# Kernel tuning notes

Hardware: AMD Instinct MI355X
Metric: run time of the kernel (lower is better)

The kernel has to match this reference:

```python
import jax, jax.numpy as jnp
import numpy as np

B, N, IN_D = 4, 2046, 512
D, H = 1024, 16
DH = D // H  # 64
S = N + 2
EPS = 1e-5


def setup_inputs() -> dict:
    key = jax.random.key(0)
    ks = jax.random.split(key, 9)
    s = lambda k, shp, fan: jax.random.normal(k, shp, jnp.float32) * (1.0 / np.sqrt(fan))
    return {
        "x": jax.random.normal(ks[0], (B, N, IN_D), jnp.float32),
        "W_map": s(ks[1], (IN_D, D), IN_D),
        "b_map": jnp.zeros((D,), jnp.float32),
        "time_token": jax.random.normal(ks[2], (1, D), jnp.float32),
        "cluster_token": jax.random.normal(ks[3], (1, D), jnp.float32),
        "ln_g": jnp.ones((D,), jnp.float32),
        "ln_b": jnp.zeros((D,), jnp.float32),
        "Wq": s(ks[4], (H, DH, DH), DH),
        "bq": jax.random.normal(ks[5], (H, DH), jnp.float32) * 0.01,
        "Wk": s(ks[6], (H, DH, DH), DH),
        "bk": jax.random.normal(ks[7], (H, DH), jnp.float32) * 0.01,
    }


def reference(x, W_map, b_map, time_token, cluster_token, ln_g, ln_b, Wq, bq, Wk, bk):
    b = x.shape[0]
    tokens = x @ W_map + b_map                       # [B, N, D]
    tt = jnp.broadcast_to(time_token[None], (b, 1, D))
    ct = jnp.broadcast_to(cluster_token[None], (b, 1, D))
    out = jnp.concatenate([tt, ct, tokens], axis=1)  # [B, S, D]
    # LayerNorm (norm1)
    mu = jnp.mean(out, axis=-1, keepdims=True)
    var = jnp.mean(jnp.square(out - mu), axis=-1, keepdims=True)
    h = (out - mu) * jax.lax.rsqrt(var + EPS) * ln_g + ln_b
    # MSAAttention: per-head Q/K linear, softmax(QK^T / sqrt(d_head))
    hh = h.reshape(b, S, H, DH)
    q = jnp.einsum("bshd,hde->bhse", hh, Wq) + bq[None, :, None, :]
    k = jnp.einsum("bshd,hde->bhse", hh, Wk) + bk[None, :, None, :]
    scores = jnp.einsum("bhse,bhte->bhst", q, k) / np.sqrt(DH).astype(np.float32)
    attn = jax.nn.softmax(scores, axis=-1)           # [B, H, S, S]
    # hstack over heads -> [B, S, H*S]; extract_attention reshapes back and
    # means over heads, then takes rows 0 (timing) and 1 (id).
    m = jnp.mean(attn, axis=1)                       # [B, S, S]
    return m[:, 0, :], m[:, 1, :]
```

## Files before the change

kernel.cpp:

```cpp
#include <hip/hip_runtime.h>
#include <hip/hip_bf16.h>
#include <math.h>

#define BB 4
#define NN 2046
#define IND 512
#define DD 1024
#define HH 16
#define SS 2048
#define MM (BB*NN)
#define MPAD 8192
#define ROWPAD 8256
#define EPSV 1e-5f

#define OFF_U    0
#define OFF_G    2048
#define OFF_C2   2080
#define OFF_S12  4096
#define OFF_A    (4096 + 2*ROWPAD)
#define OFF_XH_B  1139200
#define OFF_WHT_B (OFF_XH_B + MPAD*IND*2)
#define OFF_WLT_B (OFF_WHT_B + DD*IND*2)

typedef float f32x4 __attribute__((ext_vector_type(4)));
typedef __bf16 bf16x8 __attribute__((ext_vector_type(8)));
typedef unsigned short u16x8 __attribute__((ext_vector_type(8)));

__device__ __forceinline__ unsigned short f2bf_rne(float f) {
  unsigned int u = __float_as_uint(f);
  u += 0x7FFFu + ((u >> 16) & 1u);
  return (unsigned short)(u >> 16);
}

__device__ __forceinline__ float waveSum(float v) {
  #pragma unroll
  for (int m = 32; m >= 1; m >>= 1) v += __shfl_xor(v, m, 64);
  return v;
}

__device__ __forceinline__ float blockReduceSum(float v, volatile float* buf4) {
  #pragma unroll
  for (int m = 32; m >= 1; m >>= 1) v += __shfl_xor(v, m, 64);
  int wid = threadIdx.x >> 6;
  __syncthreads();
  if ((threadIdx.x & 63) == 0) buf4[wid] = v;
  __syncthreads();
  return buf4[0] + buf4[1] + buf4[2] + buf4[3];
}

#define GLOAD_LDS16(g, l) \
  __builtin_amdgcn_global_load_lds((const __attribute__((address_space(1))) void*)(g), \
                                   (__attribute__((address_space(3))) void*)(l), 16, 0, 0)

__global__ __launch_bounds__(256) void prep(
    const float* __restrict__ x, const float* __restrict__ Wm,
    const float* __restrict__ tt, const float* __restrict__ ct,
    const float* __restrict__ lng, const float* __restrict__ lnb,
    const float* __restrict__ Wq, const float* __restrict__ bq,
    const float* __restrict__ Wk, const float* __restrict__ bk,
    unsigned short* __restrict__ xh, unsigned short* __restrict__ wht,
    unsigned short* __restrict__ wlt, float* __restrict__ ws,
    float* __restrict__ out) {
  __shared__ float tile[64][65];
  __shared__ float hq[4][64];
  __shared__ float qs[4][64];
  const int bid = blockIdx.x;
  const int t = threadIdx.x;

  if (bid < 2048) {
    const int row = bid * 4 + (t >> 6);
    const int c0 = (t & 63) * 8;
    const size_t po = (size_t)row * IND + c0;
    u16x8 hv;
    if (row < MM) {
      const float4* xv = (const float4*)(x + po);
      float4 a = xv[0], b = xv[1];
      float vv[8] = {a.x, a.y, a.z, a.w, b.x, b.y, b.z, b.w};
      #pragma unroll
      for (int i = 0; i < 8; ++i) hv[i] = f2bf_rne(vv[i]);
    } else {
      #pragma unroll
      for (int i = 0; i < 8; ++i) hv[i] = 0;
    }
    *(u16x8*)(xh + po) = hv;
  } else if (bid < 2176) {
    const int b2 = bid - 2048;
    const int kb = b2 >> 4, nb = b2 & 15;
    const int k0 = kb * 64, n0 = nb * 64;
    #pragma unroll
    for (int q = 0; q < 16; ++q) {
      int lin = q * 256 + t;
      int kk = lin >> 6, nn = lin & 63;
      tile[kk][nn] = Wm[(size_t)(k0 + kk) * DD + n0 + nn];
    }
    __syncthreads();
    #pragma unroll
    for (int q = 0; q < 16; ++q) {
      int lin = q * 256 + t;
      int nn = lin >> 6, kk = lin & 63;
      float v = tile[kk][nn];
      unsigned short hh = f2bf_rne(v);
      wht[(size_t)(n0 + nn) * IND + k0 + kk] = hh;
      wlt[(size_t)(n0 + nn) * IND + k0 + kk] =
          f2bf_rne(v - __uint_as_float(((unsigned int)hh) << 16));
    }
  } else if (bid < 2184) {
    const int w = t >> 6, e = t & 63;
    const int sh = (bid - 2176) * 4 + w;
    const int s = sh >> 4, h = sh & 15;
    const float* src = s ? ct : tt;
    float* U   = ws + OFF_U;
    float* s12 = ws + OFF_S12;
    float* Ap  = ws + OFF_A;

    float s1 = 0.f, s2 = 0.f;
    #pragma unroll
    for (int i = 0; i < 16; ++i) { float v = src[i*64 + e]; s1 += v; s2 += v*v; }
    s1 = waveSum(s1); s2 = waveSum(s2);
    if (h == 0 && e == 0) {
      s12[(MPAD + s)*2 + 0] = s1;
      s12[(MPAD + s)*2 + 1] = s2;
    }
    const float mu = s1 * (1.f/DD);
    const float var = s2 * (1.f/DD) - mu*mu;
    const float rstd = rsqrtf(var + EPSV);
    const int d0 = h * 64;
    hq[w][e] = (src[d0+e] - mu) * rstd * lng[d0+e] + lnb[d0+e];
    float qv = bq[d0+e];
    #pragma unroll 8
    for (int d = 0; d < 64; ++d) qv += hq[w][d] * Wq[(size_t)(d0+d)*64 + e];
    qs[w][e] = qv;
    float wt = 0.f;
    #pragma unroll 8
    for (int ee = 0; ee < 64; ++ee) wt += Wk[(size_t)(d0+e)*64 + ee] * qs[w][ee];
    wt *= 0.125f;
    const float c = waveSum(qs[w][e] * bk[d0+e]) * 0.125f;
    const float u = lng[d0+e] * wt;
    U[s*DD + d0 + e] = u;
    const float G  = waveSum(lng[d0+e] * wt);
    const float C  = waveSum(lnb[d0+e] * wt);
    const float a0 = waveSum(tt[d0+e] * u);
    const float a1 = waveSum(ct[d0+e] * u);
    if (e == 0) {
      ws[OFF_G  + sh] = G;
      ws[OFF_C2 + sh] = C + c;
      Ap[(size_t)sh*ROWPAD + MPAD + 0] = a0;
      Ap[(size_t)sh*ROWPAD + MPAD + 1] = a1;
    }
  } else if (bid < 2252) {
    const int j = (bid - 2184) * 4096 + t * 16;
    const float4 z = make_float4(0.f, 0.f, 0.f, 0.f);
    #pragma unroll
    for (int q = 0; q < 4; ++q) {
      const int f = j + q * 4;
      if (f < 16384) {
        *(float4*)(ws + OFF_S12 + f) = z;
      } else {
        const int g = f - 16384;
        const int sl = g >> 13, rw = g & 8191;
        *(float4*)(ws + OFF_A + (size_t)sl*ROWPAD + rw) = z;
      }
    }
  } else {
    const int f = (bid - 2252) * 4096 + t * 16;
    const float4 z = make_float4(0.f, 0.f, 0.f, 0.f);
    #pragma unroll
    for (int q = 0; q < 4; ++q) *(float4*)(out + f + q*4) = z;
  }
}

__global__ __launch_bounds__(256, 2) void stageB(
    const unsigned short* __restrict__ xh,
    const unsigned short* __restrict__ wht, const unsigned short* __restrict__ wlt,
    const float* __restrict__ bmap, float* __restrict__ ws) {
  __shared__ unsigned short Ash[128*64], Bsh[128*64], Bsl[128*64];
  __shared__ float s12w[4][64][2];
  __shared__ float aw[4][64][2];
  const int t = threadIdx.x, wave = t >> 6, lane = t & 63;
  const int lj = lane & 15, lg = lane >> 4;
  const int mb = blockIdx.x & 63, nb = blockIdx.x >> 6;
  const int m0 = mb * 128, n0 = nb * 128;
  const int wr = wave >> 1, wc = wave & 1;
  const float* U = ws + OFF_U;
  float* s12 = ws + OFF_S12;
  float* Ap  = ws + OFF_A;

  f32x4 acc[4][4];
  #pragma unroll
  for (int i = 0; i < 4; ++i)
    #pragma unroll
    for (int j = 0; j < 4; ++j) acc[i][j] = (f32x4){0.f,0.f,0.f,0.f};

  const int rr = lane >> 3;
  const int slot = (lane & 7) ^ rr;

  for (int ks = 0; ks < 8; ++ks) {
    const size_t kofs = (size_t)ks * 64;
    #pragma unroll
    for (int q = 0; q < 4; ++q) {
      const int r = wave*32 + q*8 + rr;
      const size_t go = (size_t)(m0 + r)*IND + kofs + slot*8;
      const size_t gn = (size_t)(n0 + r)*IND + kofs + slot*8;
      const int lo = (wave*32 + q*8) * 64;
      GLOAD_LDS16(xh  + go, Ash + lo);
      GLOAD_LDS16(wht + gn, Bsh + lo);
      GLOAD_LDS16(wlt + gn, Bsl + lo);
    }
    __syncthreads();
    #pragma unroll
    for (int kf = 0; kf < 2; ++kf) {
      const int sl = kf*4 + lg;
      bf16x8 afh[4], bfh[4], bfl[4];
      #pragma unroll
      for (int i = 0; i < 4; ++i) {
        const int r = wr*64 + i*16 + lj;
        const int byt = r*128 + ((sl ^ (r & 7)) * 16);
        afh[i] = *(const bf16x8*)((const char*)Ash + byt);
      }
      #pragma unroll
      for (int j = 0; j < 4; ++j) {
        const int r = wc*64 + j*16 + lj;
        const int byt = r*128 + ((sl ^ (r & 7)) * 16);
        bfh[j] = *(const bf16x8*)((const char*)Bsh + byt);
        bfl[j] = *(const bf16x8*)((const char*)Bsl + byt);
      }
      #pragma unroll
      for (int i = 0; i < 4; ++i)
        #pragma unroll
        for (int j = 0; j < 4; ++j) {
          acc[i][j] = __builtin_amdgcn_mfma_f32_16x16x32_bf16(afh[i], bfh[j], acc[i][j], 0, 0, 0);
          acc[i][j] = __builtin_amdgcn_mfma_f32_16x16x32_bf16(afh[i], bfl[j], acc[i][j], 0, 0, 0);
        }
    }
    __syncthreads();
  }

  float s1p[16], s2p[16], a0p[16], a1p[16];
  #pragma unroll
  for (int p = 0; p < 16; ++p) { s1p[p]=0.f; s2p[p]=0.f; a0p[p]=0.f; a1p[p]=0.f; }
  #pragma unroll
  for (int j = 0; j < 4; ++j) {
    const int gc = n0 + wc*64 + j*16 + lj;
    const float bmv = bmap[gc];
    const float u0 = U[gc], u1 = U[DD + gc];
    #pragma unroll
    for (int i = 0; i < 4; ++i)
      #pragma unroll
      for (int r = 0; r < 4; ++r) {
        const float tok = acc[i][j][r] + bmv;
        const int p = i*4 + r;
        s1p[p] += tok; s2p[p] += tok*tok;
        a0p[p] += tok*u0; a1p[p] += tok*u1;
      }
  }
  #pragma unroll
  for (int msk = 8; msk >= 1; msk >>= 1)
    #pragma unroll
    for (int p = 0; p < 16; ++p) {
      s1p[p] += __shfl_xor(s1p[p], msk, 64);
      s2p[p] += __shfl_xor(s2p[p], msk, 64);
      a0p[p] += __shfl_xor(a0p[p], msk, 64);
      a1p[p] += __shfl_xor(a1p[p], msk, 64);
    }
  if (lj == 0) {
    #pragma unroll
    for (int p = 0; p < 16; ++p) {
      const int rl = (p>>2)*16 + lg*4 + (p&3);
      s12w[wave][rl][0] = s1p[p];
      s12w[wave][rl][1] = s2p[p];
      aw[wave][rl][0]   = a0p[p];
      aw[wave][rl][1]   = a1p[p];
    }
  }
  __syncthreads();
  if (t < 128) {
    const int rloc = t, wrg = rloc >> 6, rw = rloc & 63;
    const int grow = m0 + rloc;
    const int h0 = n0 >> 6;
    atomicAdd(&s12[grow*2+0], s12w[wrg*2+0][rw][0] + s12w[wrg*2+1][rw][0]);
    atomicAdd(&s12[grow*2+1], s12w[wrg*2+0][rw][1] + s12w[wrg*2+1][rw][1]);
    atomicAdd(&Ap[(size_t)(0*16 + h0    )*ROWPAD + grow], aw[wrg*2+0][rw][0]);
    atomicAdd(&Ap[(size_t)(1*16 + h0    )*ROWPAD + grow], aw[wrg*2+0][rw][1]);
    atomicAdd(&Ap[(size_t)(0*16 + h0 + 1)*ROWPAD + grow], aw[wrg*2+1][rw][0]);
    atomicAdd(&Ap[(size_t)(1*16 + h0 + 1)*ROWPAD + grow], aw[wrg*2+1][rw][1]);
  }
}

__global__ __launch_bounds__(256) void stageC1(const float* __restrict__ ws,
                                               float* __restrict__ out) {
  __shared__ float rbuf[4];
  const int bid = blockIdx.x;
  const int h = bid & 15, bs = bid >> 4, b = bs >> 1, s = bs & 1;
  const int t = threadIdx.x;
  const float* s12 = ws + OFF_S12;
  const float* Ah  = ws + OFF_A + (size_t)(s*16+h)*ROWPAD;
  const float Gh = ws[OFF_G + s*16+h], Ch = ws[OFF_C2 + s*16+h];

  float v[8];
  float sum = 0.f;
  #pragma unroll
  for (int i = 0; i < 8; ++i) {
    const int p = i*256 + t;
    const int r = (p == 0) ? MPAD : (p == 1) ? (MPAD+1) : (b*NN + p - 2);
    const float s1 = s12[r*2], s2 = s12[r*2+1];
    const float mu = s1 * (1.f/DD);
    const float var = s2 * (1.f/DD) - mu*mu;
    const float rstd = rsqrtf(var + EPSV);
    const float sc = fminf(rstd * (Ah[r] - mu*Gh) + Ch, 60.f);
    v[i] = __expf(sc);
    sum += v[i];
  }
  sum = blockReduceSum(sum, rbuf);
  const float inv = 1.f / (16.f * sum);
  float* op = out + (size_t)s*(BB*SS) + (size_t)b*SS;
  #pragma unroll
  for (int i = 0; i < 8; ++i) atomicAdd(&op[i*256 + t], v[i] * inv);
}

extern "C" void kernel_launch(void* const* d_in, const int* in_sizes, int n_in,
                              void* d_out, int out_size, void* d_ws, size_t ws_size,
                              hipStream_t stream) {
  const float* x   = (const float*)d_in[0];
  const float* Wm  = (const float*)d_in[1];
  const float* bm  = (const float*)d_in[2];
  const float* tt  = (const float*)d_in[3];
  const float* ct  = (const float*)d_in[4];
  const float* lng = (const float*)d_in[5];
  const float* lnb = (const float*)d_in[6];
  const float* Wq  = (const float*)d_in[7];
  const float* bq  = (const float*)d_in[8];
  const float* Wk  = (const float*)d_in[9];
  const float* bk  = (const float*)d_in[10];
  char* wsb = (char*)d_ws;
  float* ws = (float*)d_ws;
  float* out = (float*)d_out;

  unsigned short* xh  = (unsigned short*)(wsb + OFF_XH_B);
  unsigned short* wht = (unsigned short*)(wsb + OFF_WHT_B);
  unsigned short* wlt = (unsigned short*)(wsb + OFF_WLT_B);

  hipLaunchKernelGGL(prep,    dim3(2256), dim3(256), 0, stream,
                     x, Wm, tt, ct, lng, lnb, Wq, bq, Wk, bk,
                     xh, wht, wlt, ws, out);
  hipLaunchKernelGGL(stageB,  dim3(512),  dim3(256), 0, stream,
                     xh, wht, wlt, bm, ws);
  hipLaunchKernelGGL(stageC1, dim3(128),  dim3(256), 0, stream, ws, out);
}
```

Before: 114.2 us.

## Double-buffer GEMM loads and replace atomics with partial-sum slots and extra softmax pass

The stageB GEMM now uses a K-step of 32 with double-buffered LDS staging and explicit vmcnt waits, so global-to-LDS loads for the next step overlap the MFMAs on the current one. Row moments and head projections are written to dedicated per-column-block slots instead of being accumulated with atomics, which removes the zeroing blocks from prep. The final softmax is split into a denominator kernel and an output kernel that writes each result directly, with no atomic accumulation into a zeroed output. The cost is one more kernel launch and the exponentials being computed twice.

```diff
diff --git a/kernel.cpp b/kernel.cpp
--- a/kernel.cpp
+++ b/kernel.cpp
@@ -6,21 +6,22 @@
 #define NN 2046
 #define IND 512
 #define DD 1024
-#define HH 16
 #define SS 2048
 #define MM (BB*NN)
 #define MPAD 8192
-#define ROWPAD 8256
+#define RPAD 8256
 #define EPSV 1e-5f
 
-#define OFF_U    0
-#define OFF_G    2048
-#define OFF_C2   2080
-#define OFF_S12  4096
-#define OFF_A    (4096 + 2*ROWPAD)
-#define OFF_XH_B  1139200
-#define OFF_WHT_B (OFF_XH_B + MPAD*IND*2)
-#define OFF_WLT_B (OFF_WHT_B + DD*IND*2)
+#define F_U      0
+#define F_G      2048
+#define F_C2     2080
+#define F_SSPEC  2112
+#define F_DEN    2116
+#define F_S12    4096
+#define F_A      135168
+#define B_XH   1597440
+#define B_WHT  9986048
+#define B_WLT  11034624
 
 typedef float f32x4 __attribute__((ext_vector_type(4)));
 typedef __bf16 bf16x8 __attribute__((ext_vector_type(8)));
@@ -31,13 +32,14 @@
   u += 0x7FFFu + ((u >> 16) & 1u);
   return (unsigned short)(u >> 16);
 }
-
+__device__ __forceinline__ float bf2f(unsigned short h) {
+  return __uint_as_float(((unsigned int)h) << 16);
+}
 __device__ __forceinline__ float waveSum(float v) {
   #pragma unroll
   for (int m = 32; m >= 1; m >>= 1) v += __shfl_xor(v, m, 64);
   return v;
 }
-
 __device__ __forceinline__ float blockReduceSum(float v, volatile float* buf4) {
   #pragma unroll
   for (int m = 32; m >= 1; m >>= 1) v += __shfl_xor(v, m, 64);
@@ -59,13 +61,11 @@
     const float* __restrict__ Wq, const float* __restrict__ bq,
     const float* __restrict__ Wk, const float* __restrict__ bk,
     unsigned short* __restrict__ xh, unsigned short* __restrict__ wht,
-    unsigned short* __restrict__ wlt, float* __restrict__ ws,
-    float* __restrict__ out) {
+    unsigned short* __restrict__ wlt, float* __restrict__ ws) {
   __shared__ float tile[64][65];
   __shared__ float hq[4][64];
   __shared__ float qs[4][64];
-  const int bid = blockIdx.x;
-  const int t = threadIdx.x;
+  const int bid = blockIdx.x, t = threadIdx.x;
 
   if (bid < 2048) {
     const int row = bid * 4 + (t >> 6);
@@ -101,25 +101,21 @@
       float v = tile[kk][nn];
       unsigned short hh = f2bf_rne(v);
       wht[(size_t)(n0 + nn) * IND + k0 + kk] = hh;
-      wlt[(size_t)(n0 + nn) * IND + k0 + kk] =
-          f2bf_rne(v - __uint_as_float(((unsigned int)hh) << 16));
-    }
-  } else if (bid < 2184) {
+      wlt[(size_t)(n0 + nn) * IND + k0 + kk] = f2bf_rne(v - bf2f(hh));
+    }
+  } else {
     const int w = t >> 6, e = t & 63;
     const int sh = (bid - 2176) * 4 + w;
     const int s = sh >> 4, h = sh & 15;
     const float* src = s ? ct : tt;
-    float* U   = ws + OFF_U;
-    float* s12 = ws + OFF_S12;
-    float* Ap  = ws + OFF_A;
 
     float s1 = 0.f, s2 = 0.f;
     #pragma unroll
     for (int i = 0; i < 16; ++i) { float v = src[i*64 + e]; s1 += v; s2 += v*v; }
     s1 = waveSum(s1); s2 = waveSum(s2);
     if (h == 0 && e == 0) {
-      s12[(MPAD + s)*2 + 0] = s1;
-      s12[(MPAD + s)*2 + 1] = s2;
+      ws[F_SSPEC + s*2 + 0] = s1;
+      ws[F_SSPEC + s*2 + 1] = s2;
     }
     const float mu = s1 * (1.f/DD);
     const float var = s2 * (1.f/DD) - mu*mu;
@@ -136,36 +132,17 @@
     wt *= 0.125f;
     const float c = waveSum(qs[w][e] * bk[d0+e]) * 0.125f;
     const float u = lng[d0+e] * wt;
-    U[s*DD + d0 + e] = u;
+    ws[F_U + s*DD + d0 + e] = u;
     const float G  = waveSum(lng[d0+e] * wt);
     const float C  = waveSum(lnb[d0+e] * wt);
     const float a0 = waveSum(tt[d0+e] * u);
     const float a1 = waveSum(ct[d0+e] * u);
     if (e == 0) {
-      ws[OFF_G  + sh] = G;
-      ws[OFF_C2 + sh] = C + c;
-      Ap[(size_t)sh*ROWPAD + MPAD + 0] = a0;
-      Ap[(size_t)sh*ROWPAD + MPAD + 1] = a1;
-    }
-  } else if (bid < 2252) {
-    const int j = (bid - 2184) * 4096 + t * 16;
-    const float4 z = make_float4(0.f, 0.f, 0.f, 0.f);
-    #pragma unroll
-    for (int q = 0; q < 4; ++q) {
-      const int f = j + q * 4;
-      if (f < 16384) {
-        *(float4*)(ws + OFF_S12 + f) = z;
-      } else {
-        const int g = f - 16384;
-        const int sl = g >> 13, rw = g & 8191;
-        *(float4*)(ws + OFF_A + (size_t)sl*ROWPAD + rw) = z;
-      }
-    }
-  } else {
-    const int f = (bid - 2252) * 4096 + t * 16;
-    const float4 z = make_float4(0.f, 0.f, 0.f, 0.f);
-    #pragma unroll
-    for (int q = 0; q < 4; ++q) *(float4*)(out + f + q*4) = z;
+      ws[F_G  + sh] = G;
+      ws[F_C2 + sh] = C + c;
+      ws[F_A + (size_t)sh*RPAD + MPAD + 0] = a0;
+      ws[F_A + (size_t)sh*RPAD + MPAD + 1] = a1;
+    }
   }
 }
 
@@ -173,17 +150,13 @@
     const unsigned short* __restrict__ xh,
     const unsigned short* __restrict__ wht, const unsigned short* __restrict__ wlt,
     const float* __restrict__ bmap, float* __restrict__ ws) {
-  __shared__ unsigned short Ash[128*64], Bsh[128*64], Bsl[128*64];
-  __shared__ float s12w[4][64][2];
-  __shared__ float aw[4][64][2];
+  __shared__ char smem[49152];
   const int t = threadIdx.x, wave = t >> 6, lane = t & 63;
   const int lj = lane & 15, lg = lane >> 4;
   const int mb = blockIdx.x & 63, nb = blockIdx.x >> 6;
   const int m0 = mb * 128, n0 = nb * 128;
   const int wr = wave >> 1, wc = wave & 1;
-  const float* U = ws + OFF_U;
-  float* s12 = ws + OFF_S12;
-  float* Ap  = ws + OFF_A;
+  const float* U = ws + F_U;
 
   f32x4 acc[4][4];
   #pragma unroll
@@ -191,49 +164,66 @@
     #pragma unroll
     for (int j = 0; j < 4; ++j) acc[i][j] = (f32x4){0.f,0.f,0.f,0.f};
 
-  const int rr = lane >> 3;
-  const int slot = (lane & 7) ^ rr;
-
-  for (int ks = 0; ks < 8; ++ks) {
-    const size_t kofs = (size_t)ks * 64;
-    #pragma unroll
-    for (int q = 0; q < 4; ++q) {
-      const int r = wave*32 + q*8 + rr;
-      const size_t go = (size_t)(m0 + r)*IND + kofs + slot*8;
-      const size_t gn = (size_t)(n0 + r)*IND + kofs + slot*8;
-      const int lo = (wave*32 + q*8) * 64;
-      GLOAD_LDS16(xh  + go, Ash + lo);
-      GLOAD_LDS16(wht + gn, Bsh + lo);
-      GLOAD_LDS16(wlt + gn, Bsl + lo);
-    }
-    __syncthreads();
-    #pragma unroll
-    for (int kf = 0; kf < 2; ++kf) {
-      const int sl = kf*4 + lg;
-      bf16x8 afh[4], bfh[4], bfl[4];
+  const int srow = lane >> 2;
+  const int gslot = (lane & 3) ^ (srow & 3);
+
+  #define STAGE(ks, buf) do {                                                  \
+    const size_t ko_ = (size_t)(ks)*32 + gslot*8;                              \
+    _Pragma("unroll")                                                          \
+    for (int q = 0; q < 2; ++q) {                                              \
+      const int rb = wave*32 + q*16;                                           \
+      GLOAD_LDS16(xh  + (size_t)(m0 + rb + srow)*IND + ko_,                    \
+                  smem + (buf)*8192 + rb*64);                                  \
+      GLOAD_LDS16(wht + (size_t)(n0 + rb + srow)*IND + ko_,                    \
+                  smem + 16384 + (buf)*16384 + rb*64);                         \
+      GLOAD_LDS16(wlt + (size_t)(n0 + rb + srow)*IND + ko_,                    \
+                  smem + 16384 + (buf)*16384 + 8192 + rb*64);                  \
+    }                                                                          \
+  } while (0)
+
+  STAGE(0, 0);
+  #pragma unroll
+  for (int k = 0; k < 16; ++k) {
+    if (k < 15) {
+      STAGE(k + 1, (k + 1) & 1);
+      asm volatile("s_waitcnt vmcnt(6)" ::: "memory");
+    } else {
+      asm volatile("s_waitcnt vmcnt(0)" ::: "memory");
+    }
+    __builtin_amdgcn_sched_barrier(0);
+    __builtin_amdgcn_s_barrier();
+    __builtin_amdgcn_sched_barrier(0);
+    {
+      const int ab = (k & 1) * 8192;
+      const int bb = 16384 + (k & 1) * 16384;
+      bf16x8 af[4], bfh[4], bfl[4];
       #pragma unroll
       for (int i = 0; i < 4; ++i) {
         const int r = wr*64 + i*16 + lj;
-        const int byt = r*128 + ((sl ^ (r & 7)) * 16);
-        afh[i] = *(const bf16x8*)((const char*)Ash + byt);
+        af[i] = *(const bf16x8*)(smem + ab + r*64 + ((lg ^ (r & 3)) * 16));
       }
       #pragma unroll
       for (int j = 0; j < 4; ++j) {
         const int r = wc*64 + j*16 + lj;
-        const int byt = r*128 + ((sl ^ (r & 7)) * 16);
-        bfh[j] = *(const bf16x8*)((const char*)Bsh + byt);
-        bfl[j] = *(const bf16x8*)((const char*)Bsl + byt);
+        const int byt = r*64 + ((lg ^ (r & 3)) * 16);
+        bfh[j] = *(const bf16x8*)(smem + bb + byt);
+        bfl[j] = *(const bf16x8*)(smem + bb + 8192 + byt);
       }
       #pragma unroll
       for (int i = 0; i < 4; ++i)
         #pragma unroll
         for (int j = 0; j < 4; ++j) {
-          acc[i][j] = __builtin_amdgcn_mfma_f32_16x16x32_bf16(afh[i], bfh[j], acc[i][j], 0, 0, 0);
-          acc[i][j] = __builtin_amdgcn_mfma_f32_16x16x32_bf16(afh[i], bfl[j], acc[i][j], 0, 0, 0);
+          acc[i][j] = __builtin_amdgcn_mfma_f32_16x16x32_bf16(af[i], bfh[j], acc[i][j], 0,0,0);
+          acc[i][j] = __builtin_amdgcn_mfma_f32_16x16x32_bf16(af[i], bfl[j], acc[i][j], 0,0,0);
         }
     }
-    __syncthreads();
-  }
+    __builtin_amdgcn_sched_barrier(0);
+    asm volatile("s_waitcnt lgkmcnt(0)" ::: "memory");
+    __builtin_amdgcn_sched_barrier(0);
+    __builtin_amdgcn_s_barrier();
+    __builtin_amdgcn_sched_barrier(0);
+  }
+  #undef STAGE
 
   float s1p[16], s2p[16], a0p[16], a1p[16];
   #pragma unroll
@@ -262,59 +252,100 @@
       a0p[p] += __shfl_xor(a0p[p], msk, 64);
       a1p[p] += __shfl_xor(a1p[p], msk, 64);
     }
+
+  if (lj == 0) {
+    const int h = nb*2 + wc;
+    #pragma unroll
+    for (int p = 0; p < 16; ++p) {
+      const int row = m0 + wr*64 + (p>>2)*16 + lg*4 + (p&3);
+      ws[F_A + (size_t)h*RPAD + row]        = a0p[p];
+      ws[F_A + (size_t)(16 + h)*RPAD + row] = a1p[p];
+    }
+  }
+
+  float* s12w = (float*)smem;
   if (lj == 0) {
     #pragma unroll
     for (int p = 0; p < 16; ++p) {
       const int rl = (p>>2)*16 + lg*4 + (p&3);
-      s12w[wave][rl][0] = s1p[p];
-      s12w[wave][rl][1] = s2p[p];
-      aw[wave][rl][0]   = a0p[p];
-      aw[wave][rl][1]   = a1p[p];
+      s12w[(wave*64 + rl)*2 + 0] = s1p[p];
+      s12w[(wave*64 + rl)*2 + 1] = s2p[p];
     }
   }
   __syncthreads();
   if (t < 128) {
-    const int rloc = t, wrg = rloc >> 6, rw = rloc & 63;
-    const int grow = m0 + rloc;
-    const int h0 = n0 >> 6;
-    atomicAdd(&s12[grow*2+0], s12w[wrg*2+0][rw][0] + s12w[wrg*2+1][rw][0]);
-    atomicAdd(&s12[grow*2+1], s12w[wrg*2+0][rw][1] + s12w[wrg*2+1][rw][1]);
-    atomicAdd(&Ap[(size_t)(0*16 + h0    )*ROWPAD + grow], aw[wrg*2+0][rw][0]);
-    atomicAdd(&Ap[(size_t)(1*16 + h0    )*ROWPAD + grow], aw[wrg*2+0][rw][1]);
-    atomicAdd(&Ap[(size_t)(0*16 + h0 + 1)*ROWPAD + grow], aw[wrg*2+1][rw][0]);
-    atomicAdd(&Ap[(size_t)(1*16 + h0 + 1)*ROWPAD + grow], aw[wrg*2+1][rw][1]);
-  }
-}
-
-__global__ __launch_bounds__(256) void stageC1(const float* __restrict__ ws,
-                                               float* __restrict__ out) {
+    const int wv = t >> 6, rl = t & 63;
+    const float s1 = s12w[((wv*2)*64 + rl)*2]     + s12w[((wv*2+1)*64 + rl)*2];
+    const float s2 = s12w[((wv*2)*64 + rl)*2 + 1] + s12w[((wv*2+1)*64 + rl)*2 + 1];
+    ws[F_S12 + (size_t)(m0 + t)*16 + nb*2 + 0] = s1;
+    ws[F_S12 + (size_t)(m0 + t)*16 + nb*2 + 1] = s2;
+  }
+}
+
+__device__ __forceinline__ void rowMoments(const float* __restrict__ ws, int p,
+                                           int r, float& mu, float& rstd) {
+  float s1, s2;
+  if (p < 2) {
+    s1 = ws[F_SSPEC + p*2 + 0];
+    s2 = ws[F_SSPEC + p*2 + 1];
+  } else {
+    const float4* q4 = (const float4*)(ws + F_S12 + (size_t)r*16);
+    const float4 a = q4[0], b = q4[1], c = q4[2], d = q4[3];
+    s1 = (a.x + a.z) + (b.x + b.z) + (c.x + c.z) + (d.x + d.z);
+    s2 = (a.y + a.w) + (b.y + b.w) + (c.y + c.w) + (d.y + d.w);
+  }
+  mu = s1 * (1.f/DD);
+  const float var = s2 * (1.f/DD) - mu*mu;
+  rstd = rsqrtf(var + EPSV);
+}
+
+__global__ __launch_bounds__(256) void stageC1(float* __restrict__ ws) {
   __shared__ float rbuf[4];
   const int bid = blockIdx.x;
-  const int h = bid & 15, bs = bid >> 4, b = bs >> 1, s = bs & 1;
+  const int b = bid >> 5, sh = bid & 31;
   const int t = threadIdx.x;
-  const float* s12 = ws + OFF_S12;
-  const float* Ah  = ws + OFF_A + (size_t)(s*16+h)*ROWPAD;
-  const float Gh = ws[OFF_G + s*16+h], Ch = ws[OFF_C2 + s*16+h];
-
-  float v[8];
+  const float Gh = ws[F_G + sh], Ch = ws[F_C2 + sh];
+  const float* Af = ws + F_A + (size_t)sh*RPAD;
+
   float sum = 0.f;
   #pragma unroll
   for (int i = 0; i < 8; ++i) {
     const int p = i*256 + t;
-    const int r = (p == 0) ? MPAD : (p == 1) ? (MPAD+1) : (b*NN + p - 2);
-    const float s1 = s12[r*2], s2 = s12[r*2+1];
-    const float mu = s1 * (1.f/DD);
-    const float var = s2 * (1.f/DD) - mu*mu;
-    const float rstd = rsqrtf(var + EPSV);
-    const float sc = fminf(rstd * (Ah[r] - mu*Gh) + Ch, 60.f);
-    v[i] = __expf(sc);
-    sum += v[i];
+    const int r = (p < 2) ? (MPAD + p) : (b*NN + p - 2);
+    float mu, rstd;
+    rowMoments(ws, p, r, mu, rstd);
+    const float sc = fminf(rstd*(Af[r] - mu*Gh) + Ch, 60.f);
+    sum += __expf(sc);
   }
   sum = blockReduceSum(sum, rbuf);
-  const float inv = 1.f / (16.f * sum);
-  float* op = out + (size_t)s*(BB*SS) + (size_t)b*SS;
-  #pragma unroll
-  for (int i = 0; i < 8; ++i) atomicAdd(&op[i*256 + t], v[i] * inv);
+  if (t == 0) ws[F_DEN + bid] = sum;
+}
+
+__global__ __launch_bounds__(256) void stageC2(const float* __restrict__ ws,
+                                               float* __restrict__ out) {
+  __shared__ float dn[16], Gs[16], Cs[16];
+  const int bid = blockIdx.x;
+  const int bs = bid >> 3, chunk = bid & 7;
+  const int b = bs >> 1, s = bs & 1;
+  const int t = threadIdx.x;
+  if (t < 16) {
+    dn[t] = 1.f / ws[F_DEN + b*32 + s*16 + t];
+    Gs[t] = ws[F_G  + s*16 + t];
+    Cs[t] = ws[F_C2 + s*16 + t];
+  }
+  __syncthreads();
+  const int p = chunk*256 + t;
+  const int r = (p < 2) ? (MPAD + p) : (b*NN + p - 2);
+  float mu, rstd;
+  rowMoments(ws, p, r, mu, rstd);
+  float acc = 0.f;
+  #pragma unroll
+  for (int h = 0; h < 16; ++h) {
+    const float a = ws[F_A + (size_t)(s*16 + h)*RPAD + r];
+    const float sc = fminf(rstd*(a - mu*Gs[h]) + Cs[h], 60.f);
+    acc += __expf(sc) * dn[h];
+  }
+  out[(size_t)s*(BB*SS) + (size_t)b*SS + p] = acc * (1.f/16.f);
 }
 
 extern "C" void kernel_launch(void* const* d_in, const int* in_sizes, int n_in,
@@ -335,14 +366,14 @@
   float* ws = (float*)d_ws;
   float* out = (float*)d_out;
 
-  unsigned short* xh  = (unsigned short*)(wsb + OFF_XH_B);
-  unsigned short* wht = (unsigned short*)(wsb + OFF_WHT_B);
-  unsigned short* wlt = (unsigned short*)(wsb + OFF_WLT_B);
-
-  hipLaunchKernelGGL(prep,    dim3(2256), dim3(256), 0, stream,
-                     x, Wm, tt, ct, lng, lnb, Wq, bq, Wk, bk,
-                     xh, wht, wlt, ws, out);
+  unsigned short* xh  = (unsigned short*)(wsb + B_XH);
+  unsigned short* wht = (unsigned short*)(wsb + B_WHT);
+  unsigned short* wlt = (unsigned short*)(wsb + B_WLT);
+
+  hipLaunchKernelGGL(prep,    dim3(2184), dim3(256), 0, stream,
+                     x, Wm, tt, ct, lng, lnb, Wq, bq, Wk, bk, xh, wht, wlt, ws);
   hipLaunchKernelGGL(stageB,  dim3(512),  dim3(256), 0, stream,
                      xh, wht, wlt, bm, ws);
-  hipLaunchKernelGGL(stageC1, dim3(128),  dim3(256), 0, stream, ws, out);
-}
+  hipLaunchKernelGGL(stageC1, dim3(128),  dim3(256), 0, stream, ws);
+  hipLaunchKernelGGL(stageC2, dim3(64),   dim3(256), 0, stream, ws, out);
+}
```

Result: slower. 119.7 us (+4.8%).
